# Kernel optimization log

Measured on AMD Instinct MI355X. Metric: run time of the kernel, lower is better.

The kernel has to match this reference:

```python
import jax, jax.numpy as jnp
import numpy as np

QMAX = 255.0  # uint8 range used by KVQuantizer


def setup_inputs() -> dict:
    key = jax.random.key(0)
    k1, k2 = jax.random.split(key)
    B, KVH, D, S = 1, 8, 128, 8192
    keys = jax.random.normal(k1, (B, KVH, 1, D, S), dtype=jnp.float32)
    values = jax.random.normal(k2, (B, KVH, 1, S, D), dtype=jnp.float32)
    return {"keys": keys, "values": values, "mask": 1, "ids_len": S, "kv_seq_len": S}


def _quantize_block(x, axis):
    # torch.aminmax(x, dim=axis, keepdim=True)
    block_min = jnp.min(x, axis=axis, keepdims=True)
    block_max = jnp.max(x, axis=axis, keepdims=True)
    scale = (block_max - block_min) * (1.0 / QMAX)
    x_packed = jnp.round((x - block_min) / scale)  # F16 path: stays float
    # USE_FLOAT16_SCALE_BIAS=True -> half precision scale/bias
    return x_packed, scale.astype(jnp.float16), block_min.astype(jnp.float16)


def reference(keys, values, mask, ids_len, kv_seq_len):
    # causal mask: (1 - tril(ones)) * -128, sliced [:ids_len, :kv_seq_len], * mask, .float()
    row = jnp.arange(ids_len)[:, None]
    col = jnp.arange(kv_seq_len)[None, :]
    attn = (jnp.where(col > row, jnp.int32(-128), jnp.int32(0)) * jnp.int32(mask)).astype(jnp.float32)
    attn = attn[None, None, None]  # [1,1,1,ids_len,kv_seq_len]

    # per-layer KV-cache quantization (keys blocked over head_dim axis -2, values over -1)
    k_packed, k_scale, k_bias = _quantize_block(keys, -2)
    v_packed, v_scale, v_bias = _quantize_block(values, -1)
    return (attn, k_packed, k_scale, k_bias, v_packed, jnp.swapaxes(v_scale, -1, -2), v_bias)
```

## Files before the change

kernel.cpp:

```cpp
#include <hip/hip_runtime.h>
#include <hip/hip_fp16.h>

#define HH 8
#define DD 128
#define SS 8192

#define KEYS_BLOCKS 256
#define VALS_BLOCKS 4096
#define ATTN_BLOCKS 4096

typedef float nfloat4 __attribute__((ext_vector_type(4)));

__global__ __launch_bounds__(512) void fused_kernel(
    const float* __restrict__ keys, const float* __restrict__ vals,
    const int* __restrict__ maskp,
    float* __restrict__ attn, float* __restrict__ kp, float* __restrict__ ks,
    float* __restrict__ kb, float* __restrict__ vp, float* __restrict__ vs,
    float* __restrict__ vbias)
{
    const int bid = blockIdx.x;
    const int tid = threadIdx.x;

    __shared__ float4 smin[8][64], smax[8][64];
    __shared__ float4 sbias[64], sinv[64];

    if (bid < KEYS_BLOCKS) {
        const int h   = bid >> 5;
        const int s04 = (bid & 31) << 6;
        const int l   = tid & 63;
        const int w   = tid >> 6;
        const float4* k4 = (const float4*)keys;

        float4 val[16];
        float4 mn4 = make_float4(3e38f, 3e38f, 3e38f, 3e38f);
        float4 mx4 = make_float4(-3e38f, -3e38f, -3e38f, -3e38f);
#pragma unroll
        for (int j = 0; j < 16; ++j) {
            float4 v = k4[(size_t)(h * DD + w * 16 + j) * (SS / 4) + s04 + l];
            val[j] = v;
            mn4.x = fminf(mn4.x, v.x); mn4.y = fminf(mn4.y, v.y);
            mn4.z = fminf(mn4.z, v.z); mn4.w = fminf(mn4.w, v.w);
            mx4.x = fmaxf(mx4.x, v.x); mx4.y = fmaxf(mx4.y, v.y);
            mx4.z = fmaxf(mx4.z, v.z); mx4.w = fmaxf(mx4.w, v.w);
        }
        smin[w][l] = mn4;
        smax[w][l] = mx4;
        __syncthreads();
        if (w == 0) {
            float4 m = smin[0][l], M = smax[0][l];
#pragma unroll
            for (int i = 1; i < 8; ++i) {
                float4 a = smin[i][l], b = smax[i][l];
                m.x = fminf(m.x, a.x); m.y = fminf(m.y, a.y);
                m.z = fminf(m.z, a.z); m.w = fminf(m.w, a.w);
                M.x = fmaxf(M.x, b.x); M.y = fmaxf(M.y, b.y);
                M.z = fmaxf(M.z, b.z); M.w = fmaxf(M.w, b.w);
            }
            float4 sc;
            sc.x = (M.x - m.x) * (1.0f / 255.0f); sc.y = (M.y - m.y) * (1.0f / 255.0f);
            sc.z = (M.z - m.z) * (1.0f / 255.0f); sc.w = (M.w - m.w) * (1.0f / 255.0f);
            float4 kso, kbo;
            kso.x = __half2float(__float2half(sc.x)); kso.y = __half2float(__float2half(sc.y));
            kso.z = __half2float(__float2half(sc.z)); kso.w = __half2float(__float2half(sc.w));
            kbo.x = __half2float(__float2half(m.x)); kbo.y = __half2float(__float2half(m.y));
            kbo.z = __half2float(__float2half(m.z)); kbo.w = __half2float(__float2half(m.w));
            ((float4*)ks)[h * (SS / 4) + s04 + l] = kso;
            ((float4*)kb)[h * (SS / 4) + s04 + l] = kbo;
            float4 inv;
            inv.x = 1.0f / sc.x; inv.y = 1.0f / sc.y;
            inv.z = 1.0f / sc.z; inv.w = 1.0f / sc.w;
            sbias[l] = m;
            sinv[l]  = inv;
        }
        __syncthreads();
        const float4 b4 = sbias[l];
        const float4 i4 = sinv[l];
        float4* o4 = (float4*)kp;
#pragma unroll
        for (int j = 0; j < 16; ++j) {
            float4 o;
            o.x = rintf((val[j].x - b4.x) * i4.x);
            o.y = rintf((val[j].y - b4.y) * i4.y);
            o.z = rintf((val[j].z - b4.z) * i4.z);
            o.w = rintf((val[j].w - b4.w) * i4.w);
            o4[(size_t)(h * DD + w * 16 + j) * (SS / 4) + s04 + l] = o;
        }
    } else if (bid < KEYS_BLOCKS + VALS_BLOCKS) {
        const int vbd = bid - KEYS_BLOCKS;
        const int d4  = tid & 31;
        const int rr  = tid >> 5;
        const int R   = vbd * 16 + rr;

        const float4 v = ((const float4*)vals)[R * 32 + d4];
        float mn = fminf(fminf(v.x, v.y), fminf(v.z, v.w));
        float mx = fmaxf(fmaxf(v.x, v.y), fmaxf(v.z, v.w));
#pragma unroll
        for (int off = 16; off >= 1; off >>= 1) {
            mn = fminf(mn, __shfl_xor(mn, off));
            mx = fmaxf(mx, __shfl_xor(mx, off));
        }
        const float scale = (mx - mn) * (1.0f / 255.0f);
        const float inv = 1.0f / scale;
        if (d4 == 0) {
            vs[R]    = __half2float(__float2half(scale));
            vbias[R] = __half2float(__float2half(mn));
        }
        float4 o;
        o.x = rintf((v.x - mn) * inv);
        o.y = rintf((v.y - mn) * inv);
        o.z = rintf((v.z - mn) * inv);
        o.w = rintf((v.w - mn) * inv);
        ((float4*)vp)[R * 32 + d4] = o;
    } else {
        const int ab = bid - (KEYS_BLOCKS + VALS_BLOCKS);
        const float hi = (float)(-128 * (*maskp));
        const int base = ab * 4096 + tid;
        nfloat4* o4 = (nfloat4*)attn;
#pragma unroll
        for (int k2 = 0; k2 < 8; ++k2) {
            int idx = base + k2 * 512;
            int r = idx >> 11;
            int c = (idx & 2047) << 2;
            nfloat4 v;
            v.x = (c + 0 > r) ? hi : 0.0f;
            v.y = (c + 1 > r) ? hi : 0.0f;
            v.z = (c + 2 > r) ? hi : 0.0f;
            v.w = (c + 3 > r) ? hi : 0.0f;
            __builtin_nontemporal_store(v, &o4[idx]);
        }
    }
}

extern "C" void kernel_launch(void* const* d_in, const int* in_sizes, int n_in,
                              void* d_out, int out_size, void* d_ws, size_t ws_size,
                              hipStream_t stream) {
    const float* keys  = (const float*)d_in[0];
    const float* vals  = (const float*)d_in[1];
    const int*   maskp = (const int*)d_in[2];

    float* out  = (float*)d_out;
    float* attn = out;
    float* kp   = attn + 67108864;
    float* ks   = kp   + 8388608;
    float* kb   = ks   + 65536;
    float* vp   = kb   + 65536;
    float* vs   = vp   + 8388608;
    float* vbv  = vs   + 65536;

    const int grid = KEYS_BLOCKS + VALS_BLOCKS + ATTN_BLOCKS;
    fused_kernel<<<dim3(grid), dim3(512), 0, stream>>>(
        keys, vals, maskp, attn, kp, ks, kb, vp, vs, vbv);
}
```

Before: 384.2 us.

## Split fused kernel into separate keys, values and attention-mask kernels

Replaces the single heterogeneous fused kernel with three launches: keys quantization, values quantization with smaller 256-thread blocks, and a row-per-block causal-mask writer. The mask writer now uses ordinary stores instead of nontemporal stores. The split removes branch divergence between block types and lets each kernel use its own block size. In exchange it adds two extra launches, serializes the phases on one stream, and loses the overlap of different work types across CUs.

```diff
diff --git a/kernel.cpp b/kernel.cpp
--- a/kernel.cpp
+++ b/kernel.cpp
@@ -5,130 +5,122 @@
 #define DD 128
 #define SS 8192
 
-#define KEYS_BLOCKS 256
-#define VALS_BLOCKS 4096
-#define ATTN_BLOCKS 4096
+__global__ __launch_bounds__(256) void attn_kernel(const int* __restrict__ maskp,
+                                                   float* __restrict__ out) {
+    const float hi = (float)(-128 * (*maskp));
+    const int r = blockIdx.x;
+    float4* row = (float4*)out + (size_t)r * (SS / 4);
+    const int t = threadIdx.x;
+#pragma unroll
+    for (int k = 0; k < 8; ++k) {
+        const int f4 = k * 256 + t;
+        const int c = f4 << 2;
+        float4 v;
+        v.x = (c     > r) ? hi : 0.0f;
+        v.y = (c + 1 > r) ? hi : 0.0f;
+        v.z = (c + 2 > r) ? hi : 0.0f;
+        v.w = (c + 3 > r) ? hi : 0.0f;
+        row[f4] = v;
+    }
+}
 
-typedef float nfloat4 __attribute__((ext_vector_type(4)));
-
-__global__ __launch_bounds__(512) void fused_kernel(
-    const float* __restrict__ keys, const float* __restrict__ vals,
-    const int* __restrict__ maskp,
-    float* __restrict__ attn, float* __restrict__ kp, float* __restrict__ ks,
-    float* __restrict__ kb, float* __restrict__ vp, float* __restrict__ vs,
-    float* __restrict__ vbias)
-{
-    const int bid = blockIdx.x;
-    const int tid = threadIdx.x;
+__global__ __launch_bounds__(512) void keys_kernel(const float* __restrict__ keys,
+                                                   float* __restrict__ kp,
+                                                   float* __restrict__ ks,
+                                                   float* __restrict__ kb) {
+    const int h   = blockIdx.x >> 5;
+    const int s04 = (blockIdx.x & 31) << 6;
+    const int l   = threadIdx.x & 63;
+    const int w   = threadIdx.x >> 6;
+    const float4* k4 = (const float4*)keys;
 
     __shared__ float4 smin[8][64], smax[8][64];
     __shared__ float4 sbias[64], sinv[64];
 
-    if (bid < KEYS_BLOCKS) {
-        const int h   = bid >> 5;
-        const int s04 = (bid & 31) << 6;
-        const int l   = tid & 63;
-        const int w   = tid >> 6;
-        const float4* k4 = (const float4*)keys;
+    float4 val[16];
+    float4 mn4 = make_float4(3e38f, 3e38f, 3e38f, 3e38f);
+    float4 mx4 = make_float4(-3e38f, -3e38f, -3e38f, -3e38f);
+#pragma unroll
+    for (int j = 0; j < 16; ++j) {
+        float4 v = k4[(size_t)(h * DD + w * 16 + j) * (SS / 4) + s04 + l];
+        val[j] = v;
+        mn4.x = fminf(mn4.x, v.x); mn4.y = fminf(mn4.y, v.y);
+        mn4.z = fminf(mn4.z, v.z); mn4.w = fminf(mn4.w, v.w);
+        mx4.x = fmaxf(mx4.x, v.x); mx4.y = fmaxf(mx4.y, v.y);
+        mx4.z = fmaxf(mx4.z, v.z); mx4.w = fmaxf(mx4.w, v.w);
+    }
+    smin[w][l] = mn4;
+    smax[w][l] = mx4;
+    __syncthreads();
+    if (w == 0) {
+        float4 m = smin[0][l], M = smax[0][l];
+#pragma unroll
+        for (int i = 1; i < 8; ++i) {
+            float4 a = smin[i][l], b = smax[i][l];
+            m.x = fminf(m.x, a.x); m.y = fminf(m.y, a.y);
+            m.z = fminf(m.z, a.z); m.w = fminf(m.w, a.w);
+            M.x = fmaxf(M.x, b.x); M.y = fmaxf(M.y, b.y);
+            M.z = fmaxf(M.z, b.z); M.w = fmaxf(M.w, b.w);
+        }
+        float4 sc;
+        sc.x = (M.x - m.x) * (1.0f / 255.0f); sc.y = (M.y - m.y) * (1.0f / 255.0f);
+        sc.z = (M.z - m.z) * (1.0f / 255.0f); sc.w = (M.w - m.w) * (1.0f / 255.0f);
+        float4 kso, kbo;
+        kso.x = __half2float(__float2half(sc.x)); kso.y = __half2float(__float2half(sc.y));
+        kso.z = __half2float(__float2half(sc.z)); kso.w = __half2float(__float2half(sc.w));
+        kbo.x = __half2float(__float2half(m.x)); kbo.y = __half2float(__float2half(m.y));
+        kbo.z = __half2float(__float2half(m.z)); kbo.w = __half2float(__float2half(m.w));
+        ((float4*)ks)[h * (SS / 4) + s04 + l] = kso;
+        ((float4*)kb)[h * (SS / 4) + s04 + l] = kbo;
+        float4 inv;
+        inv.x = 1.0f / sc.x; inv.y = 1.0f / sc.y;
+        inv.z = 1.0f / sc.z; inv.w = 1.0f / sc.w;
+        sbias[l] = m;
+        sinv[l]  = inv;
+    }
+    __syncthreads();
+    const float4 b4 = sbias[l];
+    const float4 i4 = sinv[l];
+    float4* o4 = (float4*)kp;
+#pragma unroll
+    for (int j = 0; j < 16; ++j) {
+        float4 o;
+        o.x = rintf((val[j].x - b4.x) * i4.x);
+        o.y = rintf((val[j].y - b4.y) * i4.y);
+        o.z = rintf((val[j].z - b4.z) * i4.z);
+        o.w = rintf((val[j].w - b4.w) * i4.w);
+        o4[(size_t)(h * DD + w * 16 + j) * (SS / 4) + s04 + l] = o;
+    }
+}
 
-        float4 val[16];
-        float4 mn4 = make_float4(3e38f, 3e38f, 3e38f, 3e38f);
-        float4 mx4 = make_float4(-3e38f, -3e38f, -3e38f, -3e38f);
+__global__ __launch_bounds__(256) void vals_kernel(const float* __restrict__ vals,
+                                                   float* __restrict__ vp,
+                                                   float* __restrict__ vs,
+                                                   float* __restrict__ vb) {
+    const int d4 = threadIdx.x & 31;
+    const int rr = threadIdx.x >> 5;
+    const int R  = blockIdx.x * 8 + rr;
+
+    const float4 v = ((const float4*)vals)[R * 32 + d4];
+    float mn = fminf(fminf(v.x, v.y), fminf(v.z, v.w));
+    float mx = fmaxf(fmaxf(v.x, v.y), fmaxf(v.z, v.w));
 #pragma unroll
-        for (int j = 0; j < 16; ++j) {
-            float4 v = k4[(size_t)(h * DD + w * 16 + j) * (SS / 4) + s04 + l];
-            val[j] = v;
-            mn4.x = fminf(mn4.x, v.x); mn4.y = fminf(mn4.y, v.y);
-            mn4.z = fminf(mn4.z, v.z); mn4.w = fminf(mn4.w, v.w);
-            mx4.x = fmaxf(mx4.x, v.x); mx4.y = fmaxf(mx4.y, v.y);
-            mx4.z = fmaxf(mx4.z, v.z); mx4.w = fmaxf(mx4.w, v.w);
-        }
-        smin[w][l] = mn4;
-        smax[w][l] = mx4;
-        __syncthreads();
-        if (w == 0) {
-            float4 m = smin[0][l], M = smax[0][l];
-#pragma unroll
-            for (int i = 1; i < 8; ++i) {
-                float4 a = smin[i][l], b = smax[i][l];
-                m.x = fminf(m.x, a.x); m.y = fminf(m.y, a.y);
-                m.z = fminf(m.z, a.z); m.w = fminf(m.w, a.w);
-                M.x = fmaxf(M.x, b.x); M.y = fmaxf(M.y, b.y);
-                M.z = fmaxf(M.z, b.z); M.w = fmaxf(M.w, b.w);
-            }
-            float4 sc;
-            sc.x = (M.x - m.x) * (1.0f / 255.0f); sc.y = (M.y - m.y) * (1.0f / 255.0f);
-            sc.z = (M.z - m.z) * (1.0f / 255.0f); sc.w = (M.w - m.w) * (1.0f / 255.0f);
-            float4 kso, kbo;
-            kso.x = __half2float(__float2half(sc.x)); kso.y = __half2float(__float2half(sc.y));
-            kso.z = __half2float(__float2half(sc.z)); kso.w = __half2float(__float2half(sc.w));
-            kbo.x = __half2float(__float2half(m.x)); kbo.y = __half2float(__float2half(m.y));
-            kbo.z = __half2float(__float2half(m.z)); kbo.w = __half2float(__float2half(m.w));
-            ((float4*)ks)[h * (SS / 4) + s04 + l] = kso;
-            ((float4*)kb)[h * (SS / 4) + s04 + l] = kbo;
-            float4 inv;
-            inv.x = 1.0f / sc.x; inv.y = 1.0f / sc.y;
-            inv.z = 1.0f / sc.z; inv.w = 1.0f / sc.w;
-            sbias[l] = m;
-            sinv[l]  = inv;
-        }
-        __syncthreads();
-        const float4 b4 = sbias[l];
-        const float4 i4 = sinv[l];
-        float4* o4 = (float4*)kp;
-#pragma unroll
-        for (int j = 0; j < 16; ++j) {
-            float4 o;
-            o.x = rintf((val[j].x - b4.x) * i4.x);
-            o.y = rintf((val[j].y - b4.y) * i4.y);
-            o.z = rintf((val[j].z - b4.z) * i4.z);
-            o.w = rintf((val[j].w - b4.w) * i4.w);
-            o4[(size_t)(h * DD + w * 16 + j) * (SS / 4) + s04 + l] = o;
-        }
-    } else if (bid < KEYS_BLOCKS + VALS_BLOCKS) {
-        const int vbd = bid - KEYS_BLOCKS;
-        const int d4  = tid & 31;
-        const int rr  = tid >> 5;
-        const int R   = vbd * 16 + rr;
-
-        const float4 v = ((const float4*)vals)[R * 32 + d4];
-        float mn = fminf(fminf(v.x, v.y), fminf(v.z, v.w));
-        float mx = fmaxf(fmaxf(v.x, v.y), fmaxf(v.z, v.w));
-#pragma unroll
-        for (int off = 16; off >= 1; off >>= 1) {
-            mn = fminf(mn, __shfl_xor(mn, off));
-            mx = fmaxf(mx, __shfl_xor(mx, off));
-        }
-        const float scale = (mx - mn) * (1.0f / 255.0f);
-        const float inv = 1.0f / scale;
-        if (d4 == 0) {
-            vs[R]    = __half2float(__float2half(scale));
-            vbias[R] = __half2float(__float2half(mn));
-        }
-        float4 o;
-        o.x = rintf((v.x - mn) * inv);
-        o.y = rintf((v.y - mn) * inv);
-        o.z = rintf((v.z - mn) * inv);
-        o.w = rintf((v.w - mn) * inv);
-        ((float4*)vp)[R * 32 + d4] = o;
-    } else {
-        const int ab = bid - (KEYS_BLOCKS + VALS_BLOCKS);
-        const float hi = (float)(-128 * (*maskp));
-        const int base = ab * 4096 + tid;
-        nfloat4* o4 = (nfloat4*)attn;
-#pragma unroll
-        for (int k2 = 0; k2 < 8; ++k2) {
-            int idx = base + k2 * 512;
-            int r = idx >> 11;
-            int c = (idx & 2047) << 2;
-            nfloat4 v;
-            v.x = (c + 0 > r) ? hi : 0.0f;
-            v.y = (c + 1 > r) ? hi : 0.0f;
-            v.z = (c + 2 > r) ? hi : 0.0f;
-            v.w = (c + 3 > r) ? hi : 0.0f;
-            __builtin_nontemporal_store(v, &o4[idx]);
-        }
+    for (int off = 16; off >= 1; off >>= 1) {
+        mn = fminf(mn, __shfl_xor(mn, off));
+        mx = fmaxf(mx, __shfl_xor(mx, off));
     }
+    const float scale = (mx - mn) * (1.0f / 255.0f);
+    const float inv = 1.0f / scale;
+    if (d4 == 0) {
+        vs[R] = __half2float(__float2half(scale));
+        vb[R] = __half2float(__float2half(mn));
+    }
+    float4 o;
+    o.x = rintf((v.x - mn) * inv);
+    o.y = rintf((v.y - mn) * inv);
+    o.z = rintf((v.z - mn) * inv);
+    o.w = rintf((v.w - mn) * inv);
+    ((float4*)vp)[R * 32 + d4] = o;
 }
 
 extern "C" void kernel_launch(void* const* d_in, const int* in_sizes, int n_in,
@@ -147,7 +139,7 @@
     float* vs   = vp   + 8388608;
     float* vbv  = vs   + 65536;
 
-    const int grid = KEYS_BLOCKS + VALS_BLOCKS + ATTN_BLOCKS;
-    fused_kernel<<<dim3(grid), dim3(512), 0, stream>>>(
-        keys, vals, maskp, attn, kp, ks, kb, vp, vs, vbv);
+    keys_kernel<<<dim3(HH * (SS / 256)), dim3(512), 0, stream>>>(keys, kp, ks, kb);
+    vals_kernel<<<dim3(HH * SS / 8), dim3(256), 0, stream>>>(vals, vp, vs, vbv);
+    attn_kernel<<<dim3(SS), dim3(256), 0, stream>>>(maskp, attn);
 }
```

After: 384.6 us. About the same (+0.1%).
